# Optimization experiments

Measured on AMD Instinct MI355X. Metric: run time of the kernel, lower is better.

The kernel has to match this reference:

```python
import jax, jax.numpy as jnp
import numpy as np

EPS = 1e-5

def ln(x, g, b):
    m = x.mean(-1, keepdims=True)
    v = x.var(-1, keepdims=True)
    return (x - m) / jnp.sqrt(v + EPS) * g + b

def setup_inputs() -> dict:
    key = jax.random.key(0)
    ks = jax.random.split(key, 16)
    def p(k, shape, fan):
        return jax.random.normal(k, shape, jnp.float32) * (1.0 / np.sqrt(fan))
    B, N, M = 4, 256, 256
    C = 256
    inp = {}
    inp["tracks"] = jax.random.normal(ks[0], (B, 1028, N), jnp.float32)
    inp["detections"] = jax.random.normal(ks[1], (B, 1028, M), jnp.float32)
    # app encoder: Linear(1024,256) -> LN -> ReLU -> Linear(256,256)
    inp["wa1"] = p(ks[2], (1024, C), 1024); inp["ba1"] = jnp.zeros((C,), jnp.float32)
    inp["gla"] = jnp.ones((C,), jnp.float32); inp["bla"] = jnp.zeros((C,), jnp.float32)
    inp["wa2"] = p(ks[3], (C, C), C); inp["ba2"] = jnp.zeros((C,), jnp.float32)
    # geo encoder: Linear(4,128) -> LN -> ReLU -> Linear(128,256)
    inp["wg1"] = p(ks[4], (4, C // 2), 4); inp["bg1"] = jnp.zeros((C // 2,), jnp.float32)
    inp["glg"] = jnp.ones((C // 2,), jnp.float32); inp["blg"] = jnp.zeros((C // 2,), jnp.float32)
    inp["wg2"] = p(ks[5], (C // 2, C), C // 2); inp["bg2"] = jnp.zeros((C,), jnp.float32)
    # fusion LayerNorm
    inp["gf"] = jnp.ones((C,), jnp.float32); inp["bf"] = jnp.zeros((C,), jnp.float32)
    # cross-attention (4 heads, head_dim 64)
    inp["wq"] = p(ks[6], (C, C), C); inp["bq"] = jnp.zeros((C,), jnp.float32)
    inp["wk"] = p(ks[7], (C, C), C); inp["bk"] = jnp.zeros((C,), jnp.float32)
    inp["wv"] = p(ks[8], (C, C), C); inp["bv"] = jnp.zeros((C,), jnp.float32)
    inp["wo"] = p(ks[9], (C, C), C); inp["bo"] = jnp.zeros((C,), jnp.float32)
    # classifier: Linear(512,128) -> ReLU -> Linear(128,1)
    inp["wc1"] = p(ks[10], (2 * C, 128), 2 * C); inp["bc1"] = jnp.zeros((128,), jnp.float32)
    inp["wc2"] = p(ks[11], (128, 1), 128); inp["bc2"] = jnp.zeros((1,), jnp.float32)
    return inp

def reference(tracks, detections, wa1, ba1, gla, bla, wa2, ba2,
              wg1, bg1, glg, blg, wg2, bg2, gf, bf,
              wq, bq, wk, bk, wv, bv, wo, bo,
              wc1, bc1, wc2, bc2):
    tr = tracks.transpose(0, 2, 1)       # (B, N, 1028)
    de = detections.transpose(0, 2, 1)   # (B, M, 1028)

    def encode(x):
        app, geo = x[..., :1024], x[..., 1024:]
        h = jax.nn.relu(ln(app @ wa1 + ba1, gla, bla)) @ wa2 + ba2
        g = jax.nn.relu(ln(geo @ wg1 + bg1, glg, blg)) @ wg2 + bg2
        return ln(h + g, gf, bf)

    t_emb = encode(tr)   # (B, N, C)
    d_emb = encode(de)   # (B, M, C)

    B, N, C = t_emb.shape
    M = d_emb.shape[1]
    H, dh = 4, C // 4

    # Cross-attention (computed in the original forward but its output is never used)
    q = (t_emb @ wq + bq).reshape(B, N, H, dh)
    k = (d_emb @ wk + bk).reshape(B, M, H, dh)
    v = (d_emb @ wv + bv).reshape(B, M, H, dh)
    att = jax.nn.softmax(jnp.einsum('bnhd,bmhd->bhnm', q, k) / jnp.sqrt(jnp.float32(dh)), axis=-1)
    attn_out = jnp.einsum('bhnm,bmhd->bnhd', att, v).reshape(B, N, C) @ wo + bo  # unused, as in original

    # Pairwise classifier. cat([t_rep, d_rep], -1) @ wc1 == t @ wc1[:C] + d @ wc1[C:]
    a = t_emb @ wc1[:C]   # (B, N, 128)
    c = d_emb @ wc1[C:]   # (B, M, 128)
    h = jax.nn.relu(a[:, :, None, :] + c[:, None, :, :] + bc1)  # (B, N, M, 128)
    logits = (h @ wc2 + bc2)[..., 0]  # (B, N, M)
    return logits
```

## Files before the change

kernel.cpp:

```cpp
#include <hip/hip_runtime.h>

#define EPS 1e-5f


__global__ __launch_bounds__(256, 4) void k_gemm1(
    const float* __restrict__ tracks, const float* __restrict__ dets,
    const float* __restrict__ wa1, float* __restrict__ part)
{
    __shared__ float xs[128 * 16];
    const int blk = blockIdx.x;
    const int rt  = blk >> 3;
    const int ksi = blk & 7;
    const int g0  = rt * 16;
    const int side = g0 >> 10, b = (g0 >> 8) & 3, n0 = g0 & 255;
    const float* xb = (side ? dets : tracks) + (size_t)b * (1028 * 256);
    const int k0 = ksi * 128;
    const int tid = threadIdx.x;
    const int w   = tid >> 6;
    const int c0  = (tid & 63) * 4;

    for (int t = tid; t < 512; t += 256) {
        int f = t >> 2, r4 = (t & 3) << 2;
        *(float4*)(xs + f * 16 + r4) =
            *(const float4*)(xb + (size_t)(k0 + f) * 256 + n0 + r4);
    }
    __syncthreads();

    float acc[4][4];
#pragma unroll
    for (int i = 0; i < 4; ++i)
#pragma unroll
        for (int j = 0; j < 4; ++j) acc[i][j] = 0.f;

    const float* wptr = wa1 + (size_t)k0 * 256 + c0;
    float4 wb[2][8];
#pragma unroll
    for (int j = 0; j < 8; ++j)
        wb[0][j] = *(const float4*)(wptr + (size_t)j * 256);

#pragma unroll
    for (int bb = 0; bb < 16; ++bb) {
        const int cur = bb & 1, nxt = cur ^ 1;
        if (bb < 15) {
#pragma unroll
            for (int j = 0; j < 8; ++j)
                wb[nxt][j] =
                    *(const float4*)(wptr + (size_t)((bb + 1) * 8 + j) * 256);
        }
#pragma unroll
        for (int j = 0; j < 8; ++j) {
            const int f = bb * 8 + j;
            float4 xv = *(const float4*)(xs + f * 16 + w * 4);
            float4 wv = wb[cur][j];
            acc[0][0] = fmaf(xv.x, wv.x, acc[0][0]);
            acc[0][1] = fmaf(xv.x, wv.y, acc[0][1]);
            acc[0][2] = fmaf(xv.x, wv.z, acc[0][2]);
            acc[0][3] = fmaf(xv.x, wv.w, acc[0][3]);
            acc[1][0] = fmaf(xv.y, wv.x, acc[1][0]);
            acc[1][1] = fmaf(xv.y, wv.y, acc[1][1]);
            acc[1][2] = fmaf(xv.y, wv.z, acc[1][2]);
            acc[1][3] = fmaf(xv.y, wv.w, acc[1][3]);
            acc[2][0] = fmaf(xv.z, wv.x, acc[2][0]);
            acc[2][1] = fmaf(xv.z, wv.y, acc[2][1]);
            acc[2][2] = fmaf(xv.z, wv.z, acc[2][2]);
            acc[2][3] = fmaf(xv.z, wv.w, acc[2][3]);
            acc[3][0] = fmaf(xv.w, wv.x, acc[3][0]);
            acc[3][1] = fmaf(xv.w, wv.y, acc[3][1]);
            acc[3][2] = fmaf(xv.w, wv.z, acc[3][2]);
            acc[3][3] = fmaf(xv.w, wv.w, acc[3][3]);
        }
    }
    float* pb = part + ((size_t)ksi * 2048 + g0 + w * 4) * 256 + c0;
#pragma unroll
    for (int i = 0; i < 4; ++i)
        *(float4*)(pb + (size_t)i * 256) =
            make_float4(acc[i][0], acc[i][1], acc[i][2], acc[i][3]);
}

__global__ __launch_bounds__(256) void k_reduce1(
    const float* __restrict__ tracks, const float* __restrict__ dets,
    const float* __restrict__ part,
    const float* __restrict__ ba1, const float* __restrict__ gla,
    const float* __restrict__ bla,
    const float* __restrict__ wg1, const float* __restrict__ bg1,
    const float* __restrict__ glg, const float* __restrict__ blg,
    float* __restrict__ h1ext)
{
    __shared__ float red[4][4][2];
    __shared__ float geo_s[4][4];
    const int blk = blockIdx.x;
    const int g0 = blk * 4;
    const int side = g0 >> 10, b = (g0 >> 8) & 3, n0 = g0 & 255;
    const float* xb = (side ? dets : tracks) + (size_t)b * (1028 * 256);
    const int tid = threadIdx.x, wave = tid >> 6, lane = tid & 63, c = tid;

    if (tid < 16)
        geo_s[tid >> 2][tid & 3] =
            xb[(size_t)(1024 + (tid & 3)) * 256 + n0 + (tid >> 2)];

    float h[4];
#pragma unroll
    for (int i = 0; i < 4; ++i) {
        float s = ba1[c];
#pragma unroll
        for (int s8 = 0; s8 < 8; ++s8)
            s += part[((size_t)s8 * 2048 + g0 + i) * 256 + c];
        h[i] = s;
    }
#pragma unroll
    for (int i = 0; i < 4; ++i) {
        float s = h[i], s2 = h[i] * h[i];
#pragma unroll
        for (int off = 32; off >= 1; off >>= 1) {
            s  += __shfl_xor(s,  off, 64);
            s2 += __shfl_xor(s2, off, 64);
        }
        if (lane == 0) { red[wave][i][0] = s; red[wave][i][1] = s2; }
    }
    __syncthreads();
    {
        float gv = gla[c], bv = bla[c];
#pragma unroll
        for (int i = 0; i < 4; ++i) {
            float s  = red[0][i][0] + red[1][i][0] + red[2][i][0] + red[3][i][0];
            float s2 = red[0][i][1] + red[1][i][1] + red[2][i][1] + red[3][i][1];
            float m   = s * (1.f / 256.f);
            float var = s2 * (1.f / 256.f) - m * m;
            h1ext[(size_t)(g0 + i) * 384 + c] =
                fmaxf((h[i] - m) * rsqrtf(var + EPS) * gv + bv, 0.f);
        }
    }
    __syncthreads();

    float gh[4];
    if (tid < 128) {
        const int j = tid;
#pragma unroll
        for (int i = 0; i < 4; ++i) {
            float s = bg1[j];
#pragma unroll
            for (int f = 0; f < 4; ++f)
                s = fmaf(geo_s[i][f], wg1[f * 128 + j], s);
            gh[i] = s;
        }
#pragma unroll
        for (int i = 0; i < 4; ++i) {
            float s = gh[i], s2 = gh[i] * gh[i];
#pragma unroll
            for (int off = 32; off >= 1; off >>= 1) {
                s  += __shfl_xor(s,  off, 64);
                s2 += __shfl_xor(s2, off, 64);
            }
            if (lane == 0) { red[wave][i][0] = s; red[wave][i][1] = s2; }
        }
    }
    __syncthreads();
    if (tid < 128) {
        const int j = tid;
        float gv = glg[j], bv = blg[j];
#pragma unroll
        for (int i = 0; i < 4; ++i) {
            float s  = red[0][i][0] + red[1][i][0];
            float s2 = red[0][i][1] + red[1][i][1];
            float m   = s * (1.f / 128.f);
            float var = s2 * (1.f / 128.f) - m * m;
            h1ext[(size_t)(g0 + i) * 384 + 256 + j] =
                fmaxf((gh[i] - m) * rsqrtf(var + EPS) * gv + bv, 0.f);
        }
    }
}

__global__ __launch_bounds__(256, 4) void k_gemm2(
    const float* __restrict__ h1ext,
    const float* __restrict__ wa2, const float* __restrict__ wg2,
    float* __restrict__ part)
{
    __shared__ float xs[64 * 16];
    const int blk = blockIdx.x;
    const int rt = blk / 6, sl = blk - rt * 6;
    const int g0 = rt * 16;
    const int k0 = sl * 64;
    const int tid = threadIdx.x;
    const int w   = tid >> 6;
    const int c0  = (tid & 63) * 4;
    const float* Wb = (k0 < 256) ? (wa2 + (size_t)k0 * 256)
                                 : (wg2 + (size_t)(k0 - 256) * 256);

    for (int idx = tid; idx < 1024; idx += 256) {
        int f = idx >> 4, r = idx & 15;
        xs[f * 16 + r] = h1ext[(size_t)(g0 + r) * 384 + k0 + f];
    }
    __syncthreads();

    float acc[4][4];
#pragma unroll
    for (int i = 0; i < 4; ++i)
#pragma unroll
        for (int j = 0; j < 4; ++j) acc[i][j] = 0.f;

    const float* wptr = Wb + c0;
    float4 wb[2][8];
#pragma unroll
    for (int j = 0; j < 8; ++j)
        wb[0][j] = *(const float4*)(wptr + (size_t)j * 256);

#pragma unroll
    for (int bb = 0; bb < 8; ++bb) {
        const int cur = bb & 1, nxt = cur ^ 1;
        if (bb < 7) {
#pragma unroll
            for (int j = 0; j < 8; ++j)
                wb[nxt][j] =
                    *(const float4*)(wptr + (size_t)((bb + 1) * 8 + j) * 256);
        }
#pragma unroll
        for (int j = 0; j < 8; ++j) {
            const int f = bb * 8 + j;
            float4 xv = *(const float4*)(xs + f * 16 + w * 4);
            float4 wv = wb[cur][j];
            acc[0][0] = fmaf(xv.x, wv.x, acc[0][0]);
            acc[0][1] = fmaf(xv.x, wv.y, acc[0][1]);
            acc[0][2] = fmaf(xv.x, wv.z, acc[0][2]);
            acc[0][3] = fmaf(xv.x, wv.w, acc[0][3]);
            acc[1][0] = fmaf(xv.y, wv.x, acc[1][0]);
            acc[1][1] = fmaf(xv.y, wv.y, acc[1][1]);
            acc[1][2] = fmaf(xv.y, wv.z, acc[1][2]);
            acc[1][3] = fmaf(xv.y, wv.w, acc[1][3]);
            acc[2][0] = fmaf(xv.z, wv.x, acc[2][0]);
            acc[2][1] = fmaf(xv.z, wv.y, acc[2][1]);
            acc[2][2] = fmaf(xv.z, wv.z, acc[2][2]);
            acc[2][3] = fmaf(xv.z, wv.w, acc[2][3]);
            acc[3][0] = fmaf(xv.w, wv.x, acc[3][0]);
            acc[3][1] = fmaf(xv.w, wv.y, acc[3][1]);
            acc[3][2] = fmaf(xv.w, wv.z, acc[3][2]);
            acc[3][3] = fmaf(xv.w, wv.w, acc[3][3]);
        }
    }
    float* pb = part + ((size_t)sl * 2048 + g0 + w * 4) * 256 + c0;
#pragma unroll
    for (int i = 0; i < 4; ++i)
        *(float4*)(pb + (size_t)i * 256) =
            make_float4(acc[i][0], acc[i][1], acc[i][2], acc[i][3]);
}

__global__ __launch_bounds__(256) void k_reduce2(
    const float* __restrict__ part,
    const float* __restrict__ ba2, const float* __restrict__ bg2,
    const float* __restrict__ gf,  const float* __restrict__ bf,
    const float* __restrict__ wc1,
    float* __restrict__ aout, float* __restrict__ cout)
{
    __shared__ float red[4][4][2];
    __shared__ float emb[256 * 4];
    __shared__ float psum[2][4][128];
    const int blk = blockIdx.x;
    const int g0 = blk * 4;
    const int side = g0 >> 10, b = (g0 >> 8) & 3, nin = g0 & 255;
    const int tid = threadIdx.x, wave = tid >> 6, lane = tid & 63, c = tid;

    float h2[4];
#pragma unroll
    for (int i = 0; i < 4; ++i) {
        float s = ba2[c] + bg2[c];
#pragma unroll
        for (int sl = 0; sl < 6; ++sl)
            s += part[((size_t)sl * 2048 + g0 + i) * 256 + c];
        h2[i] = s;
    }
#pragma unroll
    for (int i = 0; i < 4; ++i) {
        float s = h2[i], s2 = h2[i] * h2[i];
#pragma unroll
        for (int off = 32; off >= 1; off >>= 1) {
            s  += __shfl_xor(s,  off, 64);
            s2 += __shfl_xor(s2, off, 64);
        }
        if (lane == 0) { red[wave][i][0] = s; red[wave][i][1] = s2; }
    }
    __syncthreads();
    {
        float gv = gf[c], bv = bf[c];
        float e[4];
#pragma unroll
        for (int i = 0; i < 4; ++i) {
            float s  = red[0][i][0] + red[1][i][0] + red[2][i][0] + red[3][i][0];
            float s2 = red[0][i][1] + red[1][i][1] + red[2][i][1] + red[3][i][1];
            float m   = s * (1.f / 256.f);
            float var = s2 * (1.f / 256.f) - m * m;
            e[i] = (h2[i] - m) * rsqrtf(var + EPS) * gv + bv;
        }
        *(float4*)(emb + (size_t)c * 4) = make_float4(e[0], e[1], e[2], e[3]);
    }
    __syncthreads();

    const int half = tid >> 7, j = tid & 127;
    const float* wch = wc1 + (size_t)side * (256 * 128);
    float a4[4] = {0.f, 0.f, 0.f, 0.f};
#pragma unroll 4
    for (int k = 0; k < 128; ++k) {
        int kk = half * 128 + k;
        float w = wch[(size_t)kk * 128 + j];
        float4 ev = *(const float4*)(emb + kk * 4);
        a4[0] = fmaf(ev.x, w, a4[0]); a4[1] = fmaf(ev.y, w, a4[1]);
        a4[2] = fmaf(ev.z, w, a4[2]); a4[3] = fmaf(ev.w, w, a4[3]);
    }
#pragma unroll
    for (int i = 0; i < 4; ++i) psum[half][i][j] = a4[i];
    __syncthreads();

    float* outp = (side ? cout : aout) + ((size_t)b * 256 + nin) * 128;
    for (int idx = tid; idx < 512; idx += 256) {
        int i = idx >> 7, jo = idx & 127;
        outp[(size_t)i * 128 + jo] = psum[0][i][jo] + psum[1][i][jo];
    }
}

__global__ __launch_bounds__(256) void k_pairwise(
    const float* __restrict__ a, const float* __restrict__ cmat,
    const float* __restrict__ bc1, const float* __restrict__ wc2,
    const float* __restrict__ bc2, float* __restrict__ out)
{
    __shared__ float4 a_s[16 * 33];
    __shared__ float4 c_s[16 * 33];
    const int blk = blockIdx.x;
    const int b  = blk >> 8;
    const int n0 = ((blk >> 4) & 15) << 4;
    const int m0 = (blk & 15) << 4;
    const int tid = threadIdx.x;

    const float4* a4  = (const float4*)(a    + ((size_t)b * 256 + n0) * 128);
    const float4* c4  = (const float4*)(cmat + ((size_t)b * 256 + m0) * 128);
    const float4* b14 = (const float4*)bc1;
    for (int idx = tid; idx < 512; idx += 256) {
        int r = idx >> 5, q = idx & 31;
        float4 av = a4[r * 32 + q], bv = b14[q];
        a_s[r * 33 + q] = make_float4(av.x + bv.x, av.y + bv.y,
                                      av.z + bv.z, av.w + bv.w);
        c_s[r * 33 + q] = c4[r * 32 + q];
    }
    __syncthreads();

    const int ni = tid >> 4, mi = tid & 15;
    const float4* wp = (const float4*)wc2;
    float acc = bc2[0];
#pragma unroll 8
    for (int q = 0; q < 32; ++q) {
        float4 av = a_s[ni * 33 + q];
        float4 cv = c_s[mi * 33 + q];
        float4 wv = wp[q];
        acc = fmaf(fmaxf(av.x + cv.x, 0.f), wv.x, acc);
        acc = fmaf(fmaxf(av.y + cv.y, 0.f), wv.y, acc);
        acc = fmaf(fmaxf(av.z + cv.z, 0.f), wv.z, acc);
        acc = fmaf(fmaxf(av.w + cv.w, 0.f), wv.w, acc);
    }
    out[((size_t)b * 256 + n0 + ni) * 256 + m0 + mi] = acc;
}

extern "C" void kernel_launch(void* const* d_in, const int* in_sizes, int n_in,
                              void* d_out, int out_size, void* d_ws, size_t ws_size,
                              hipStream_t stream)
{
    const float* tracks = (const float*)d_in[0];
    const float* dets   = (const float*)d_in[1];
    const float* wa1 = (const float*)d_in[2];
    const float* ba1 = (const float*)d_in[3];
    const float* gla = (const float*)d_in[4];
    const float* bla = (const float*)d_in[5];
    const float* wa2 = (const float*)d_in[6];
    const float* ba2 = (const float*)d_in[7];
    const float* wg1 = (const float*)d_in[8];
    const float* bg1 = (const float*)d_in[9];
    const float* glg = (const float*)d_in[10];
    const float* blg = (const float*)d_in[11];
    const float* wg2 = (const float*)d_in[12];
    const float* bg2 = (const float*)d_in[13];
    const float* gf  = (const float*)d_in[14];
    const float* bf  = (const float*)d_in[15];
    const float* wc1 = (const float*)d_in[24];
    const float* bc1 = (const float*)d_in[25];
    const float* wc2 = (const float*)d_in[26];
    const float* bc2 = (const float*)d_in[27];
    float* out = (float*)d_out;
    float* ws  = (float*)d_ws;

    float* part  = ws;
    float* h1ext = ws + 4194304;
    float* aa    = ws + 4980736;
    float* cc    = ws + 5111808;

    hipLaunchKernelGGL(k_gemm1, dim3(1024), dim3(256), 0, stream,
                       tracks, dets, wa1, part);
    hipLaunchKernelGGL(k_reduce1, dim3(512), dim3(256), 0, stream,
                       tracks, dets, part, ba1, gla, bla,
                       wg1, bg1, glg, blg, h1ext);
    hipLaunchKernelGGL(k_gemm2, dim3(768), dim3(256), 0, stream,
                       h1ext, wa2, wg2, part);
    hipLaunchKernelGGL(k_reduce2, dim3(512), dim3(256), 0, stream,
                       part, ba2, bg2, gf, bf, wc1, aa, cc);
    hipLaunchKernelGGL(k_pairwise, dim3(1024), dim3(256), 0, stream,
                       aa, cc, bc1, wc2, bc2, out);
}
```

Measured before the change: 169.0 us.

## Fuse second encoder GEMM into reduce kernels and widen first GEMM row tile

Merges reduce1, gemm2 and reduce2 into one tail kernel. Each 4-row block keeps its hidden activations in shared memory and does the 384x256 second-layer GEMM in place, which removes two launches and the global round trips for h1ext and the split-K partials. k_gemm1 now computes 32 rows per block instead of 16, halving the grid and reusing each loaded weight vector across twice as many rows. The cost is that every tail block rereads all of wa2 and wg2 with only 4 rows of reuse, and register pressure rises in gemm1.

```diff
diff --git a/kernel.cpp b/kernel.cpp
--- a/kernel.cpp
+++ b/kernel.cpp
@@ -3,15 +3,15 @@
 #define EPS 1e-5f
 
 
-__global__ __launch_bounds__(256, 4) void k_gemm1(
+__global__ __launch_bounds__(256, 2) void k_gemm1(
     const float* __restrict__ tracks, const float* __restrict__ dets,
     const float* __restrict__ wa1, float* __restrict__ part)
 {
-    __shared__ float xs[128 * 16];
+    __shared__ __align__(16) float xs[128 * 32];
     const int blk = blockIdx.x;
     const int rt  = blk >> 3;
     const int ksi = blk & 7;
-    const int g0  = rt * 16;
+    const int g0  = rt * 32;
     const int side = g0 >> 10, b = (g0 >> 8) & 3, n0 = g0 & 255;
     const float* xb = (side ? dets : tracks) + (size_t)b * (1028 * 256);
     const int k0 = ksi * 128;
@@ -19,16 +19,16 @@
     const int w   = tid >> 6;
     const int c0  = (tid & 63) * 4;
 
-    for (int t = tid; t < 512; t += 256) {
-        int f = t >> 2, r4 = (t & 3) << 2;
-        *(float4*)(xs + f * 16 + r4) =
+    for (int t = tid; t < 1024; t += 256) {
+        int f = t >> 3, r4 = (t & 7) << 2;
+        *(float4*)(xs + f * 32 + r4) =
             *(const float4*)(xb + (size_t)(k0 + f) * 256 + n0 + r4);
     }
     __syncthreads();
 
-    float acc[4][4];
-#pragma unroll
-    for (int i = 0; i < 4; ++i)
+    float acc[8][4];
+#pragma unroll
+    for (int i = 0; i < 8; ++i)
 #pragma unroll
         for (int j = 0; j < 4; ++j) acc[i][j] = 0.f;
 
@@ -50,49 +50,51 @@
 #pragma unroll
         for (int j = 0; j < 8; ++j) {
             const int f = bb * 8 + j;
-            float4 xv = *(const float4*)(xs + f * 16 + w * 4);
+            float4 x0 = *(const float4*)(xs + f * 32 + w * 8);
+            float4 x1 = *(const float4*)(xs + f * 32 + w * 8 + 4);
             float4 wv = wb[cur][j];
-            acc[0][0] = fmaf(xv.x, wv.x, acc[0][0]);
-            acc[0][1] = fmaf(xv.x, wv.y, acc[0][1]);
-            acc[0][2] = fmaf(xv.x, wv.z, acc[0][2]);
-            acc[0][3] = fmaf(xv.x, wv.w, acc[0][3]);
-            acc[1][0] = fmaf(xv.y, wv.x, acc[1][0]);
-            acc[1][1] = fmaf(xv.y, wv.y, acc[1][1]);
-            acc[1][2] = fmaf(xv.y, wv.z, acc[1][2]);
-            acc[1][3] = fmaf(xv.y, wv.w, acc[1][3]);
-            acc[2][0] = fmaf(xv.z, wv.x, acc[2][0]);
-            acc[2][1] = fmaf(xv.z, wv.y, acc[2][1]);
-            acc[2][2] = fmaf(xv.z, wv.z, acc[2][2]);
-            acc[2][3] = fmaf(xv.z, wv.w, acc[2][3]);
-            acc[3][0] = fmaf(xv.w, wv.x, acc[3][0]);
-            acc[3][1] = fmaf(xv.w, wv.y, acc[3][1]);
-            acc[3][2] = fmaf(xv.w, wv.z, acc[3][2]);
-            acc[3][3] = fmaf(xv.w, wv.w, acc[3][3]);
-        }
-    }
-    float* pb = part + ((size_t)ksi * 2048 + g0 + w * 4) * 256 + c0;
-#pragma unroll
-    for (int i = 0; i < 4; ++i)
+            float xv[8] = {x0.x, x0.y, x0.z, x0.w, x1.x, x1.y, x1.z, x1.w};
+#pragma unroll
+            for (int i = 0; i < 8; ++i) {
+                acc[i][0] = fmaf(xv[i], wv.x, acc[i][0]);
+                acc[i][1] = fmaf(xv[i], wv.y, acc[i][1]);
+                acc[i][2] = fmaf(xv[i], wv.z, acc[i][2]);
+                acc[i][3] = fmaf(xv[i], wv.w, acc[i][3]);
+            }
+        }
+    }
+    float* pb = part + ((size_t)ksi * 2048 + g0 + w * 8) * 256 + c0;
+#pragma unroll
+    for (int i = 0; i < 8; ++i)
         *(float4*)(pb + (size_t)i * 256) =
             make_float4(acc[i][0], acc[i][1], acc[i][2], acc[i][3]);
 }
 
-__global__ __launch_bounds__(256) void k_reduce1(
+__global__ __launch_bounds__(256, 2) void k_tail(
     const float* __restrict__ tracks, const float* __restrict__ dets,
     const float* __restrict__ part,
     const float* __restrict__ ba1, const float* __restrict__ gla,
     const float* __restrict__ bla,
     const float* __restrict__ wg1, const float* __restrict__ bg1,
     const float* __restrict__ glg, const float* __restrict__ blg,
-    float* __restrict__ h1ext)
+    const float* __restrict__ wa2, const float* __restrict__ ba2,
+    const float* __restrict__ wg2, const float* __restrict__ bg2,
+    const float* __restrict__ gf,  const float* __restrict__ bf,
+    const float* __restrict__ wc1,
+    float* __restrict__ aout, float* __restrict__ cout)
 {
+    __shared__ __align__(16) float h1e[384 * 4];
+    __shared__ __align__(16) float psum[16 * 256];
+    __shared__ __align__(16) float emb[256 * 4];
+    __shared__ float ps2[2][4][128];
     __shared__ float red[4][4][2];
     __shared__ float geo_s[4][4];
+
     const int blk = blockIdx.x;
     const int g0 = blk * 4;
     const int side = g0 >> 10, b = (g0 >> 8) & 3, n0 = g0 & 255;
     const float* xb = (side ? dets : tracks) + (size_t)b * (1028 * 256);
-    const int tid = threadIdx.x, wave = tid >> 6, lane = tid & 63, c = tid;
+    const int tid = threadIdx.x, w = tid >> 6, lane = tid & 63, c = tid;
 
     if (tid < 16)
         geo_s[tid >> 2][tid & 3] =
@@ -115,7 +117,7 @@
             s  += __shfl_xor(s,  off, 64);
             s2 += __shfl_xor(s2, off, 64);
         }
-        if (lane == 0) { red[wave][i][0] = s; red[wave][i][1] = s2; }
+        if (lane == 0) { red[w][i][0] = s; red[w][i][1] = s2; }
     }
     __syncthreads();
     {
@@ -126,7 +128,7 @@
             float s2 = red[0][i][1] + red[1][i][1] + red[2][i][1] + red[3][i][1];
             float m   = s * (1.f / 256.f);
             float var = s2 * (1.f / 256.f) - m * m;
-            h1ext[(size_t)(g0 + i) * 384 + c] =
+            h1e[c * 4 + i] =
                 fmaxf((h[i] - m) * rsqrtf(var + EPS) * gv + bv, 0.f);
         }
     }
@@ -151,7 +153,7 @@
                 s  += __shfl_xor(s,  off, 64);
                 s2 += __shfl_xor(s2, off, 64);
             }
-            if (lane == 0) { red[wave][i][0] = s; red[wave][i][1] = s2; }
+            if (lane == 0) { red[w][i][0] = s; red[w][i][1] = s2; }
         }
     }
     __syncthreads();
@@ -164,107 +166,62 @@
             float s2 = red[0][i][1] + red[1][i][1];
             float m   = s * (1.f / 128.f);
             float var = s2 * (1.f / 128.f) - m * m;
-            h1ext[(size_t)(g0 + i) * 384 + 256 + j] =
+            h1e[(256 + j) * 4 + i] =
                 fmaxf((gh[i] - m) * rsqrtf(var + EPS) * gv + bv, 0.f);
         }
     }
-}
-
-__global__ __launch_bounds__(256, 4) void k_gemm2(
-    const float* __restrict__ h1ext,
-    const float* __restrict__ wa2, const float* __restrict__ wg2,
-    float* __restrict__ part)
-{
-    __shared__ float xs[64 * 16];
-    const int blk = blockIdx.x;
-    const int rt = blk / 6, sl = blk - rt * 6;
-    const int g0 = rt * 16;
-    const int k0 = sl * 64;
-    const int tid = threadIdx.x;
-    const int w   = tid >> 6;
-    const int c0  = (tid & 63) * 4;
-    const float* Wb = (k0 < 256) ? (wa2 + (size_t)k0 * 256)
-                                 : (wg2 + (size_t)(k0 - 256) * 256);
-
-    for (int idx = tid; idx < 1024; idx += 256) {
-        int f = idx >> 4, r = idx & 15;
-        xs[f * 16 + r] = h1ext[(size_t)(g0 + r) * 384 + k0 + f];
-    }
-    __syncthreads();
-
+    __syncthreads();
+
+    const int c0 = lane * 4;
     float acc[4][4];
 #pragma unroll
     for (int i = 0; i < 4; ++i)
 #pragma unroll
         for (int j = 0; j < 4; ++j) acc[i][j] = 0.f;
 
-    const float* wptr = Wb + c0;
-    float4 wb[2][8];
-#pragma unroll
-    for (int j = 0; j < 8; ++j)
-        wb[0][j] = *(const float4*)(wptr + (size_t)j * 256);
-
-#pragma unroll
-    for (int bb = 0; bb < 8; ++bb) {
-        const int cur = bb & 1, nxt = cur ^ 1;
-        if (bb < 7) {
-#pragma unroll
-            for (int j = 0; j < 8; ++j)
-                wb[nxt][j] =
-                    *(const float4*)(wptr + (size_t)((bb + 1) * 8 + j) * 256);
-        }
-#pragma unroll
-        for (int j = 0; j < 8; ++j) {
-            const int f = bb * 8 + j;
-            float4 xv = *(const float4*)(xs + f * 16 + w * 4);
-            float4 wv = wb[cur][j];
-            acc[0][0] = fmaf(xv.x, wv.x, acc[0][0]);
-            acc[0][1] = fmaf(xv.x, wv.y, acc[0][1]);
-            acc[0][2] = fmaf(xv.x, wv.z, acc[0][2]);
-            acc[0][3] = fmaf(xv.x, wv.w, acc[0][3]);
-            acc[1][0] = fmaf(xv.y, wv.x, acc[1][0]);
-            acc[1][1] = fmaf(xv.y, wv.y, acc[1][1]);
-            acc[1][2] = fmaf(xv.y, wv.z, acc[1][2]);
-            acc[1][3] = fmaf(xv.y, wv.w, acc[1][3]);
-            acc[2][0] = fmaf(xv.z, wv.x, acc[2][0]);
-            acc[2][1] = fmaf(xv.z, wv.y, acc[2][1]);
-            acc[2][2] = fmaf(xv.z, wv.z, acc[2][2]);
-            acc[2][3] = fmaf(xv.z, wv.w, acc[2][3]);
-            acc[3][0] = fmaf(xv.w, wv.x, acc[3][0]);
-            acc[3][1] = fmaf(xv.w, wv.y, acc[3][1]);
-            acc[3][2] = fmaf(xv.w, wv.z, acc[3][2]);
-            acc[3][3] = fmaf(xv.w, wv.w, acc[3][3]);
-        }
-    }
-    float* pb = part + ((size_t)sl * 2048 + g0 + w * 4) * 256 + c0;
+    {
+        const int ka = w * 64;
+#pragma unroll 4
+        for (int k = 0; k < 64; ++k) {
+            float4 xv = *(const float4*)(h1e + (ka + k) * 4);
+            float4 wv = *(const float4*)(wa2 + (size_t)(ka + k) * 256 + c0);
+#pragma unroll
+            for (int i = 0; i < 4; ++i) {
+                float x = (&xv.x)[i];
+                acc[i][0] = fmaf(x, wv.x, acc[i][0]);
+                acc[i][1] = fmaf(x, wv.y, acc[i][1]);
+                acc[i][2] = fmaf(x, wv.z, acc[i][2]);
+                acc[i][3] = fmaf(x, wv.w, acc[i][3]);
+            }
+        }
+        const int kg = w * 32;
+#pragma unroll 4
+        for (int k = 0; k < 32; ++k) {
+            float4 xv = *(const float4*)(h1e + (256 + kg + k) * 4);
+            float4 wv = *(const float4*)(wg2 + (size_t)(kg + k) * 256 + c0);
+#pragma unroll
+            for (int i = 0; i < 4; ++i) {
+                float x = (&xv.x)[i];
+                acc[i][0] = fmaf(x, wv.x, acc[i][0]);
+                acc[i][1] = fmaf(x, wv.y, acc[i][1]);
+                acc[i][2] = fmaf(x, wv.z, acc[i][2]);
+                acc[i][3] = fmaf(x, wv.w, acc[i][3]);
+            }
+        }
+    }
 #pragma unroll
     for (int i = 0; i < 4; ++i)
-        *(float4*)(pb + (size_t)i * 256) =
+        *(float4*)(psum + (w * 4 + i) * 256 + c0) =
             make_float4(acc[i][0], acc[i][1], acc[i][2], acc[i][3]);
-}
-
-__global__ __launch_bounds__(256) void k_reduce2(
-    const float* __restrict__ part,
-    const float* __restrict__ ba2, const float* __restrict__ bg2,
-    const float* __restrict__ gf,  const float* __restrict__ bf,
-    const float* __restrict__ wc1,
-    float* __restrict__ aout, float* __restrict__ cout)
-{
-    __shared__ float red[4][4][2];
-    __shared__ float emb[256 * 4];
-    __shared__ float psum[2][4][128];
-    const int blk = blockIdx.x;
-    const int g0 = blk * 4;
-    const int side = g0 >> 10, b = (g0 >> 8) & 3, nin = g0 & 255;
-    const int tid = threadIdx.x, wave = tid >> 6, lane = tid & 63, c = tid;
+    __syncthreads();
 
     float h2[4];
 #pragma unroll
     for (int i = 0; i < 4; ++i) {
         float s = ba2[c] + bg2[c];
 #pragma unroll
-        for (int sl = 0; sl < 6; ++sl)
-            s += part[((size_t)sl * 2048 + g0 + i) * 256 + c];
+        for (int w4 = 0; w4 < 4; ++w4)
+            s += psum[(w4 * 4 + i) * 256 + c];
         h2[i] = s;
     }
 #pragma unroll
@@ -275,21 +232,19 @@
             s  += __shfl_xor(s,  off, 64);
             s2 += __shfl_xor(s2, off, 64);
         }
-        if (lane == 0) { red[wave][i][0] = s; red[wave][i][1] = s2; }
+        if (lane == 0) { red[w][i][0] = s; red[w][i][1] = s2; }
     }
     __syncthreads();
     {
         float gv = gf[c], bv = bf[c];
-        float e[4];
 #pragma unroll
         for (int i = 0; i < 4; ++i) {
             float s  = red[0][i][0] + red[1][i][0] + red[2][i][0] + red[3][i][0];
             float s2 = red[0][i][1] + red[1][i][1] + red[2][i][1] + red[3][i][1];
             float m   = s * (1.f / 256.f);
             float var = s2 * (1.f / 256.f) - m * m;
-            e[i] = (h2[i] - m) * rsqrtf(var + EPS) * gv + bv;
-        }
-        *(float4*)(emb + (size_t)c * 4) = make_float4(e[0], e[1], e[2], e[3]);
+            emb[c * 4 + i] = (h2[i] - m) * rsqrtf(var + EPS) * gv + bv;
+        }
     }
     __syncthreads();
 
@@ -299,19 +254,19 @@
 #pragma unroll 4
     for (int k = 0; k < 128; ++k) {
         int kk = half * 128 + k;
-        float w = wch[(size_t)kk * 128 + j];
+        float wv = wch[(size_t)kk * 128 + j];
         float4 ev = *(const float4*)(emb + kk * 4);
-        a4[0] = fmaf(ev.x, w, a4[0]); a4[1] = fmaf(ev.y, w, a4[1]);
-        a4[2] = fmaf(ev.z, w, a4[2]); a4[3] = fmaf(ev.w, w, a4[3]);
-    }
-#pragma unroll
-    for (int i = 0; i < 4; ++i) psum[half][i][j] = a4[i];
-    __syncthreads();
-
-    float* outp = (side ? cout : aout) + ((size_t)b * 256 + nin) * 128;
+        a4[0] = fmaf(ev.x, wv, a4[0]); a4[1] = fmaf(ev.y, wv, a4[1]);
+        a4[2] = fmaf(ev.z, wv, a4[2]); a4[3] = fmaf(ev.w, wv, a4[3]);
+    }
+#pragma unroll
+    for (int i = 0; i < 4; ++i) ps2[half][i][j] = a4[i];
+    __syncthreads();
+
+    float* outp = (side ? cout : aout) + ((size_t)b * 256 + n0) * 128;
     for (int idx = tid; idx < 512; idx += 256) {
         int i = idx >> 7, jo = idx & 127;
-        outp[(size_t)i * 128 + jo] = psum[0][i][jo] + psum[1][i][jo];
+        outp[(size_t)i * 128 + jo] = ps2[0][i][jo] + ps2[1][i][jo];
     }
 }
 
@@ -383,20 +338,16 @@
     float* out = (float*)d_out;
     float* ws  = (float*)d_ws;
 
-    float* part  = ws;
-    float* h1ext = ws + 4194304;
-    float* aa    = ws + 4980736;
-    float* cc    = ws + 5111808;
-
-    hipLaunchKernelGGL(k_gemm1, dim3(1024), dim3(256), 0, stream,
+    float* part = ws;
+    float* aa   = ws + 4980736;
+    float* cc   = ws + 5111808;
+
+    hipLaunchKernelGGL(k_gemm1, dim3(512), dim3(256), 0, stream,
                        tracks, dets, wa1, part);
-    hipLaunchKernelGGL(k_reduce1, dim3(512), dim3(256), 0, stream,
+    hipLaunchKernelGGL(k_tail, dim3(512), dim3(256), 0, stream,
                        tracks, dets, part, ba1, gla, bla,
-                       wg1, bg1, glg, blg, h1ext);
-    hipLaunchKernelGGL(k_gemm2, dim3(768), dim3(256), 0, stream,
-                       h1ext, wa2, wg2, part);
-    hipLaunchKernelGGL(k_reduce2, dim3(512), dim3(256), 0, stream,
-                       part, ba2, bg2, gf, bf, wc1, aa, cc);
+                       wg1, bg1, glg, blg, wa2, ba2, wg2, bg2,
+                       gf, bf, wc1, aa, cc);
     hipLaunchKernelGGL(k_pairwise, dim3(1024), dim3(256), 0, stream,
                        aa, cc, bc1, wc2, bc2, out);
 }
```

Result: faster. 160.3 us (-5.1%).
